# Optimization experiments

Hardware: AMD Instinct MI355X
Metric: run time of the kernel (lower is better)

Reference implementation:

```python
import jax, jax.numpy as jnp
import numpy as np

N = 16384      # total atoms (8 proteins x ~2048)
E = 524288     # N * max_neighbors(32)
B = 8          # graphs
F_IN = 26      # 20 residue types + 6 atom types
D = 128        # node_dim
H = 256        # hidden_dim
OUT = 64       # output_dim
L = 4          # n_layers
N_RBF = 16
CUTOFF = 10.0


def setup_inputs() -> dict:
    key = jax.random.key(0)
    ks = jax.random.split(key, 24)
    s = 0.05
    inp = {
        "positions": jax.random.normal(ks[0], (N, 3), jnp.float32) * 10.0,
        "node_features": jax.random.normal(ks[1], (N, F_IN), jnp.float32),
        "edge_index": jax.random.randint(ks[2], (2, E), 0, N, jnp.int32),
        "batch": jnp.sort(jax.random.randint(ks[3], (N,), 0, B, jnp.int32)),
        # node embedding MLP
        "emb_W1": jax.random.normal(ks[4], (F_IN, D), jnp.float32) * s,
        "emb_b1": jnp.zeros((D,), jnp.float32),
        "emb_W2": jax.random.normal(ks[5], (D, D), jnp.float32) * s,
        "emb_b2": jnp.zeros((D,), jnp.float32),
        # per-layer message MLP: [2D + n_rbf] -> H -> D
        "msg_W1": jax.random.normal(ks[6], (L, 2 * D + N_RBF, H), jnp.float32) * s,
        "msg_b1": jnp.zeros((L, H), jnp.float32),
        "msg_W2": jax.random.normal(ks[7], (L, H, D), jnp.float32) * s,
        "msg_b2": jnp.zeros((L, D), jnp.float32),
        # per-layer update MLP: [2D] -> H -> D (residual)
        "upd_W1": jax.random.normal(ks[8], (L, 2 * D, H), jnp.float32) * s,
        "upd_b1": jnp.zeros((L, H), jnp.float32),
        "upd_W2": jax.random.normal(ks[9], (L, H, D), jnp.float32) * s,
        "upd_b2": jnp.zeros((L, D), jnp.float32),
        # readout MLP: D -> H -> OUT
        "r_W1": jax.random.normal(ks[10], (D, H), jnp.float32) * s,
        "r_b1": jnp.zeros((H,), jnp.float32),
        "r_W2": jax.random.normal(ks[11], (H, OUT), jnp.float32) * s,
        "r_b2": jnp.zeros((OUT,), jnp.float32),
    }
    return inp


def _mlp2(x, W1, b1, W2, b2):
    return jax.nn.silu(x @ W1 + b1) @ W2 + b2


def _edge_rbf(positions, src, dst):
    rel = positions[dst] - positions[src]                      # (E,3)
    d = jnp.sqrt(jnp.sum(rel * rel, axis=-1) + 1e-12)          # (E,)
    centers = jnp.linspace(0.0, CUTOFF, N_RBF, dtype=positions.dtype)
    width = CUTOFF / N_RBF
    rbf = jnp.exp(-((d[:, None] - centers) ** 2) / (2.0 * width * width))  # (E,n_rbf)
    env = 0.5 * (jnp.cos(jnp.pi * d / CUTOFF) + 1.0) * (d < CUTOFF)        # cosine cutoff
    return rbf * env[:, None]


def reference(positions, node_features, edge_index, batch,
              emb_W1, emb_b1, emb_W2, emb_b2,
              msg_W1, msg_b1, msg_W2, msg_b2,
              upd_W1, upd_b1, upd_W2, upd_b2,
              r_W1, r_b1, r_W2, r_b2):
    src, dst = edge_index[0], edge_index[1]
    h = _mlp2(node_features, emb_W1, emb_b1, emb_W2, emb_b2)   # (N,D)
    ef = _edge_rbf(positions, src, dst)                        # (E,n_rbf)
    for i in range(L):
        m_in = jnp.concatenate([h[src], h[dst], ef], axis=-1)  # (E,2D+n_rbf)
        m = _mlp2(m_in, msg_W1[i], msg_b1[i], msg_W2[i], msg_b2[i])  # (E,D)
        agg = jax.ops.segment_sum(m, dst, num_segments=N)      # (N,D)
        u_in = jnp.concatenate([h, agg], axis=-1)              # (N,2D)
        h = h + _mlp2(u_in, upd_W1[i], upd_b1[i], upd_W2[i], upd_b2[i])
    # mean readout per graph
    counts = jax.ops.segment_sum(jnp.ones((N,), h.dtype), batch, num_segments=B)
    g = jax.ops.segment_sum(h, batch, num_segments=B) / jnp.maximum(counts, 1.0)[:, None]
    return _mlp2(g, r_W1, r_b1, r_W2, r_b2)                    # (B,OUT)
```

## Files before the change

### kernel.cpp

```cpp
#include <hip/hip_runtime.h>
#include <math.h>

#define NATOMS 16384
#define NEDGES 524288
#define NLAYERS 4
#define TE 64

typedef __bf16 bf16x8 __attribute__((ext_vector_type(8)));
typedef __bf16 bf16x4 __attribute__((ext_vector_type(4)));
typedef __bf16 bf16x2 __attribute__((ext_vector_type(2)));
typedef float f32x4 __attribute__((ext_vector_type(4)));

__device__ __forceinline__ float silu_f(float x) {
  return x * __builtin_amdgcn_rcpf(1.0f + __expf(-x));
}

__global__ __launch_bounds__(256) void hist_kernel(
    const int* __restrict__ dst, int* __restrict__ counts)
{
  int e = blockIdx.x * 256 + threadIdx.x;
  atomicAdd(&counts[dst[e]], 1);
}

__global__ __launch_bounds__(1024) void scan_kernel(
    const int* __restrict__ counts, int* __restrict__ cursor,
    float* __restrict__ degf)
{
  __shared__ int s_tot[1024];
  int tid = threadIdx.x;
  int v[16];
  {
    const int4* cp = (const int4*)(counts + tid * 16);
    int4 a = cp[0], b = cp[1], c = cp[2], d = cp[3];
    v[0]=a.x; v[1]=a.y; v[2]=a.z; v[3]=a.w;
    v[4]=b.x; v[5]=b.y; v[6]=b.z; v[7]=b.w;
    v[8]=c.x; v[9]=c.y; v[10]=c.z; v[11]=c.w;
    v[12]=d.x; v[13]=d.y; v[14]=d.z; v[15]=d.w;
  }
  int tot = 0;
  #pragma unroll
  for (int i = 0; i < 16; i++) tot += v[i];
  s_tot[tid] = tot;
  __syncthreads();
  for (int off = 1; off < 1024; off <<= 1) {
    int t = (tid >= off) ? s_tot[tid - off] : 0;
    __syncthreads();
    s_tot[tid] += t;
    __syncthreads();
  }
  int run = s_tot[tid] - tot;
  #pragma unroll
  for (int i = 0; i < 16; i++) {
    cursor[tid * 16 + i] = run;
    degf[tid * 16 + i] = (float)v[i];
    run += v[i];
  }
}

__global__ __launch_bounds__(256) void scatter_kernel(
    const int* __restrict__ src, const int* __restrict__ dst,
    int* __restrict__ cursor, int* __restrict__ esrc, int* __restrict__ edst)
{
  int e = blockIdx.x * 256 + threadIdx.x;
  int d = dst[e];
  int p = atomicAdd(&cursor[d], 1);
  esrc[p] = src[e];
  edst[p] = d;
}

__global__ __launch_bounds__(256) void prep_kernel(
    const float* __restrict__ mW1, const float* __restrict__ mW2,
    const float* __restrict__ uW1, const float* __restrict__ uW2,
    const float* __restrict__ mb2,
    __bf16* __restrict__ W1at, __bf16* __restrict__ W1bt,
    __bf16* __restrict__ B2c, __bf16* __restrict__ uW1ft,
    __bf16* __restrict__ uW2t, float* __restrict__ b2u)
{
  long l = blockIdx.y;
  int bx = blockIdx.x, tid = threadIdx.x;
  if (bx < 128) {
    int i = bx * 256 + tid;
    int n = i >> 7, k = i & 127;
    W1at[l * (256L * 128) + i] = (__bf16)mW1[l * (272L * 256) + (size_t)k * 256 + n];
  } else if (bx < 256) {
    int i = (bx - 128) * 256 + tid;
    int n = i >> 7, k = i & 127;
    W1bt[l * (256L * 128) + i] = (__bf16)mW1[l * (272L * 256) + (size_t)(128 + k) * 256 + n];
  } else if (bx < 288) {
    int i = (bx - 256) * 256 + tid;
    int c = i >> 5, k = i & 31;
    float v = (k < 16) ? mW1[l * (272L * 256) + (size_t)(256 + k) * 256 + c] : 0.0f;
    B2c[l * (256L * 32) + i] = (__bf16)v;
  } else if (bx < 672) {
    int i = (bx - 288) * 256 + tid;
    int n = i / 384, k = i - n * 384;
    float v;
    if (k < 128) {
      v = uW1[l * 65536 + (size_t)k * 256 + n];
    } else {
      int r = k - 128;
      v = 0.0f;
      for (int j = 0; j < 128; j++)
        v += mW2[(l * 256 + r) * 128 + j] * uW1[l * 65536 + (size_t)(128 + j) * 256 + n];
    }
    uW1ft[l * (256L * 384) + i] = (__bf16)v;
  } else if (bx < 800) {
    int i = (bx - 672) * 256 + tid;
    int n = i >> 8, k = i & 255;
    uW2t[l * (128L * 256) + i] = (__bf16)uW2[l * (256L * 128) + (size_t)k * 128 + n];
  } else {
    int c = tid;
    float acc = 0.0f;
    for (int j = 0; j < 128; j++)
      acc += mb2[l * 128 + j] * uW1[l * 65536 + (size_t)(128 + j) * 256 + c];
    b2u[l * 256 + c] = acc;
  }
}

__global__ __launch_bounds__(128) void embed_kernel(
    const float* __restrict__ x, const float* __restrict__ W1,
    const float* __restrict__ b1, const float* __restrict__ W2,
    const float* __restrict__ b2, float* __restrict__ h,
    __bf16* __restrict__ hb)
{
  int n = blockIdx.x;
  int j = threadIdx.x;
  __shared__ float xs[26];
  __shared__ float hid[128];
  if (j < 26) xs[j] = x[n * 26 + j];
  __syncthreads();
  float acc = b1[j];
  #pragma unroll
  for (int k = 0; k < 26; k++) acc += xs[k] * W1[k * 128 + j];
  hid[j] = silu_f(acc);
  __syncthreads();
  float acc2 = b2[j];
  #pragma unroll 8
  for (int k = 0; k < 128; k++) acc2 += hid[k] * W2[k * 128 + j];
  h[(size_t)n * 128 + j] = acc2;
  hb[(size_t)n * 128 + j] = (__bf16)acc2;
}

__global__ __launch_bounds__(256) void rbf_kernel(
    const float* __restrict__ pos, const int* __restrict__ esrc,
    const int* __restrict__ edst, __bf16* __restrict__ efb)
{
  int e = blockIdx.x * 256 + threadIdx.x;
  int s = esrc[e], d = edst[e];
  float dx = pos[d * 3 + 0] - pos[s * 3 + 0];
  float dy = pos[d * 3 + 1] - pos[s * 3 + 1];
  float dz = pos[d * 3 + 2] - pos[s * 3 + 2];
  float dist = sqrtf(dx * dx + dy * dy + dz * dz + 1e-12f);
  float env = (dist < 10.0f)
                  ? 0.5f * (cosf(3.14159265358979f * dist * 0.1f) + 1.0f)
                  : 0.0f;
  bf16x8 o0, o1;
  #pragma unroll
  for (int i = 0; i < 16; i++) {
    float c = (10.0f / 15.0f) * (float)i;
    float t = dist - c;
    float v = env * __expf(-t * t * 1.28f);
    if (i < 8) o0[i] = (__bf16)v; else o1[i - 8] = (__bf16)v;
  }
  *(bf16x8*)(efb + (size_t)e * 16 + 0) = o0;
  *(bf16x8*)(efb + (size_t)e * 16 + 8) = o1;
}

__global__ __launch_bounds__(256) void zprep_kernel(
    const __bf16* __restrict__ hb, const float* __restrict__ b1,
    const __bf16* __restrict__ W1at, const __bf16* __restrict__ W1bt,
    __bf16* __restrict__ z1b, __bf16* __restrict__ z2b, float* __restrict__ aggH)
{
  __shared__ __bf16 s_n[64][136];
  int tid = threadIdx.x, n0 = blockIdx.x * 64;
  {
    int n = tid >> 2, t4 = tid & 3;
    const bf16x8* hr = (const bf16x8*)(hb + (size_t)(n0 + n) * 128);
    #pragma unroll
    for (int i = 0; i < 4; i++)
      *(bf16x8*)&s_n[n][t4 * 8 + 32 * i] = hr[t4 + 4 * i];
  }
  {
    float4 zz = make_float4(0.f, 0.f, 0.f, 0.f);
    float4* ap = (float4*)(aggH + (size_t)n0 * 256);
    for (int i = tid; i < 64 * 256 / 4; i += 256) ap[i] = zz;
  }
  __syncthreads();
  const int wv = tid >> 6, ln = tid & 63, lc = ln & 15, qd = ln >> 4;
  for (int cp = 0; cp < 2; cp++) {
    f32x4 aA[4][2], aB[4][2];
    #pragma unroll
    for (int nt = 0; nt < 2; nt++) {
      float bv = b1[cp * 128 + wv * 32 + nt * 16 + lc];
      #pragma unroll
      for (int mt = 0; mt < 4; mt++) {
        aA[mt][nt][0] = 0.f; aA[mt][nt][1] = 0.f;
        aA[mt][nt][2] = 0.f; aA[mt][nt][3] = 0.f;
        aB[mt][nt][0] = bv; aB[mt][nt][1] = bv;
        aB[mt][nt][2] = bv; aB[mt][nt][3] = bv;
      }
    }
    #pragma unroll
    for (int kt = 0; kt < 4; kt++) {
      bf16x8 af[4];
      #pragma unroll
      for (int mt = 0; mt < 4; mt++)
        af[mt] = *(const bf16x8*)&s_n[mt * 16 + lc][kt * 32 + qd * 8];
      bf16x8 bwA[2], bwB[2];
      #pragma unroll
      for (int nt = 0; nt < 2; nt++) {
        int c = cp * 128 + wv * 32 + nt * 16 + lc;
        bwA[nt] = *(const bf16x8*)(W1at + (size_t)c * 128 + kt * 32 + qd * 8);
        bwB[nt] = *(const bf16x8*)(W1bt + (size_t)c * 128 + kt * 32 + qd * 8);
      }
      #pragma unroll
      for (int mt = 0; mt < 4; mt++)
        #pragma unroll
        for (int nt = 0; nt < 2; nt++) {
          aA[mt][nt] = __builtin_amdgcn_mfma_f32_16x16x32_bf16(af[mt], bwA[nt], aA[mt][nt], 0, 0, 0);
          aB[mt][nt] = __builtin_amdgcn_mfma_f32_16x16x32_bf16(af[mt], bwB[nt], aB[mt][nt], 0, 0, 0);
        }
    }
    #pragma unroll
    for (int mt = 0; mt < 4; mt++)
      #pragma unroll
      for (int nt = 0; nt < 2; nt++) {
        int c = cp * 128 + wv * 32 + nt * 16 + lc;
        #pragma unroll
        for (int r = 0; r < 4; r++) {
          int n = n0 + mt * 16 + qd * 4 + r;
          z1b[(size_t)n * 256 + c] = (__bf16)aA[mt][nt][r];
          z2b[(size_t)n * 256 + c] = (__bf16)aB[mt][nt][r];
        }
      }
  }
}

#define MS_EF_OFF   33792
#define MS_SRC_OFF  36864
#define MS_DST_OFF  37120
#define MS_MASK_OFF 37376
#define MS_BYTES    37392

__global__ __launch_bounds__(256, 4) void msg_mfma_kernel(
    const __bf16* __restrict__ z1b, const __bf16* __restrict__ z2b,
    const __bf16* __restrict__ efb,
    const int* __restrict__ esrc, const int* __restrict__ edst,
    const __bf16* __restrict__ B2c, float* __restrict__ aggH)
{
  __shared__ __align__(16) char smem[MS_BYTES];
  __bf16 (*s_hT)[66] = (__bf16(*)[66])(smem);
  __bf16 (*s_ef)[24] = (__bf16(*)[24])(smem + MS_EF_OFF);
  int* s_src = (int*)(smem + MS_SRC_OFF);
  int* s_dst = (int*)(smem + MS_DST_OFF);
  unsigned int* s_mask = (unsigned int*)(smem + MS_MASK_OFF);

  int tid = threadIdx.x, e0 = blockIdx.x * TE;

  if (tid < TE) {
    int d = edst[e0 + tid];
    s_dst[tid] = d;
    int dp = (tid == 0) ? (d ^ 1) : edst[e0 + tid - 1];
    unsigned long long mb = __ballot(d != dp);
    if (tid == 0) { s_mask[0] = (unsigned int)mb; s_mask[1] = (unsigned int)(mb >> 32); }
  } else if (tid < 2 * TE) {
    s_src[tid - TE] = esrc[e0 + tid - TE];
  }
  {
    int e = tid >> 2, t4 = tid & 3;
    if (t4 < 2)
      *(bf16x8*)&s_ef[e][t4 * 8] =
          *(const bf16x8*)(efb + (size_t)(e0 + e) * 16 + t4 * 8);
  }
  __syncthreads();

  const int wv = tid >> 6, ln = tid & 63, lc = ln & 15, qd = ln >> 4;

  bf16x8 bI;
  #pragma unroll
  for (int j = 0; j < 8; j++)
    bI[j] = (__bf16)((lc == (qd & 1) * 8 + j) ? 1.0f : 0.0f);

  const __bf16* pz[4];
  #pragma unroll
  for (int mt = 0; mt < 4; mt++) {
    int m = mt * 16 + lc;
    int row = (qd < 2) ? s_src[m] : s_dst[m];
    pz[mt] = ((qd < 2) ? z1b : z2b) + (size_t)row * 256 + (qd & 1) * 8;
  }

  #pragma unroll
  for (int hf = 0; hf < 2; hf++) {
    const int cb = hf * 128 + wv * 32;
    bf16x8 bw[2];
    #pragma unroll
    for (int nt = 0; nt < 2; nt++)
      bw[nt] = *(const bf16x8*)(B2c + (size_t)(cb + nt * 16 + lc) * 32 + qd * 8);

    #pragma unroll
    for (int mt = 0; mt < 4; mt++) {
      bf16x8 aef = *(const bf16x8*)&s_ef[mt * 16 + lc][(qd & 1) * 8];
      #pragma unroll
      for (int nt = 0; nt < 2; nt++) {
        bf16x8 az = *(const bf16x8*)(pz[mt] + cb + nt * 16);
        f32x4 z; z[0] = 0.f; z[1] = 0.f; z[2] = 0.f; z[3] = 0.f;
        f32x4 acc = __builtin_amdgcn_mfma_f32_16x16x32_bf16(az, bI, z, 0, 0, 0);
        acc = __builtin_amdgcn_mfma_f32_16x16x32_bf16(aef, bw[nt], acc, 0, 0, 0);
        bf16x2 p0, p1;
        p0[0] = (__bf16)silu_f(acc[0]); p0[1] = (__bf16)silu_f(acc[1]);
        p1[0] = (__bf16)silu_f(acc[2]); p1[1] = (__bf16)silu_f(acc[3]);
        __bf16* wp = &s_hT[cb + nt * 16 + lc][mt * 16 + qd * 4];
        *(bf16x2*)wp = p0;
        *(bf16x2*)(wp + 2) = p1;
      }
    }
  }
  __syncthreads();

  {
    const unsigned int mlo = __builtin_amdgcn_readfirstlane(s_mask[0]);
    const unsigned int mhi = __builtin_amdgcn_readfirstlane(s_mask[1]);
    int j = tid;
    float acc = 0.0f;
    int cur = s_dst[0];
    #pragma unroll 8
    for (int i = 0; i < 64; i += 2) {
      bf16x2 p = *(const bf16x2*)&s_hT[j][i];
      bool b0 = (i < 32) ? ((mlo >> i) & 1u) : ((mhi >> (i - 32)) & 1u);
      int i1 = i + 1;
      bool b1 = (i1 < 32) ? ((mlo >> i1) & 1u) : ((mhi >> (i1 - 32)) & 1u);
      if (i > 0 && b0) {
        atomicAdd(&aggH[(size_t)cur * 256 + j], acc);
        acc = 0.0f; cur = s_dst[i];
      }
      acc += (float)p[0];
      if (b1) {
        atomicAdd(&aggH[(size_t)cur * 256 + j], acc);
        acc = 0.0f; cur = s_dst[i1];
      }
      acc += (float)p[1];
    }
    atomicAdd(&aggH[(size_t)cur * 256 + j], acc);
  }
}

__global__ __launch_bounds__(256, 2) void upd_mfma_kernel(
    float* __restrict__ h, __bf16* __restrict__ hb,
    float* __restrict__ aggH, const float* __restrict__ degf,
    const __bf16* __restrict__ uW1ft, const float* __restrict__ b1,
    const float* __restrict__ b2u,
    const __bf16* __restrict__ uW2t, const float* __restrict__ b2,
    int do_z, const float* __restrict__ nb1,
    const __bf16* __restrict__ nW1at, const __bf16* __restrict__ nW1bt,
    __bf16* __restrict__ z1b, __bf16* __restrict__ z2b)
{
  __shared__ __bf16 s_u[64][392];
  __shared__ __bf16 s_uh[64][136];
  int tid = threadIdx.x, n0 = blockIdx.x * 64;
  {
    int n = tid >> 2, t4 = tid & 3;
    const bf16x8* hr = (const bf16x8*)(hb + (size_t)(n0 + n) * 128);
    #pragma unroll
    for (int i = 0; i < 4; i++)
      *(bf16x8*)&s_u[n][t4 * 8 + 32 * i] = hr[t4 + 4 * i];
    const float* sr = aggH + (size_t)(n0 + n) * 256;
    #pragma unroll
    for (int i = 0; i < 8; i++) {
      int col = t4 * 8 + i * 32;
      float4 a = *(const float4*)(sr + col);
      float4 b = *(const float4*)(sr + col + 4);
      bf16x8 o;
      o[0] = (__bf16)a.x; o[1] = (__bf16)a.y; o[2] = (__bf16)a.z; o[3] = (__bf16)a.w;
      o[4] = (__bf16)b.x; o[5] = (__bf16)b.y; o[6] = (__bf16)b.z; o[7] = (__bf16)b.w;
      *(bf16x8*)&s_u[n][128 + col] = o;
    }
  }
  __syncthreads();
  const int wv = tid >> 6, ln = tid & 63, lc = ln & 15, qd = ln >> 4;

  float dg[4][4];
  #pragma unroll
  for (int mt = 0; mt < 4; mt++)
    #pragma unroll
    for (int r = 0; r < 4; r++)
      dg[mt][r] = degf[n0 + mt * 16 + qd * 4 + r];

  f32x4 acc2[4][2];
  #pragma unroll
  for (int nt = 0; nt < 2; nt++) {
    float bv = b2[wv * 32 + nt * 16 + lc];
    #pragma unroll
    for (int mt = 0; mt < 4; mt++) {
      acc2[mt][nt][0] = bv; acc2[mt][nt][1] = bv;
      acc2[mt][nt][2] = bv; acc2[mt][nt][3] = bv;
    }
  }

  for (int hf = 0; hf < 2; hf++) {
    f32x4 acc1[4][2];
    #pragma unroll
    for (int nt = 0; nt < 2; nt++) {
      int c = hf * 128 + wv * 32 + nt * 16 + lc;
      float bv = b1[c];
      float b2uv = b2u[c];
      #pragma unroll
      for (int mt = 0; mt < 4; mt++)
        #pragma unroll
        for (int r = 0; r < 4; r++)
          acc1[mt][nt][r] = bv + dg[mt][r] * b2uv;
    }
    #pragma unroll
    for (int kt = 0; kt < 12; kt++) {
      bf16x8 af[4];
      #pragma unroll
      for (int mt = 0; mt < 4; mt++)
        af[mt] = *(const bf16x8*)&s_u[mt * 16 + lc][kt * 32 + qd * 8];
      bf16x8 bw[2];
      #pragma unroll
      for (int nt = 0; nt < 2; nt++)
        bw[nt] = *(const bf16x8*)(uW1ft +
                 (size_t)(hf * 128 + wv * 32 + nt * 16 + lc) * 384 + kt * 32 + qd * 8);
      #pragma unroll
      for (int mt = 0; mt < 4; mt++)
        #pragma unroll
        for (int nt = 0; nt < 2; nt++)
          acc1[mt][nt] = __builtin_amdgcn_mfma_f32_16x16x32_bf16(af[mt], bw[nt], acc1[mt][nt], 0, 0, 0);
    }
    __syncthreads();
    #pragma unroll
    for (int mt = 0; mt < 4; mt++)
      #pragma unroll
      for (int nt = 0; nt < 2; nt++) {
        int cc = wv * 32 + nt * 16 + lc;
        #pragma unroll
        for (int r = 0; r < 4; r++)
          s_uh[mt * 16 + qd * 4 + r][cc] = (__bf16)silu_f(acc1[mt][nt][r]);
      }
    __syncthreads();
    #pragma unroll
    for (int kt = 0; kt < 4; kt++) {
      bf16x8 a2[4];
      #pragma unroll
      for (int mt = 0; mt < 4; mt++)
        a2[mt] = *(const bf16x8*)&s_uh[mt * 16 + lc][kt * 32 + qd * 8];
      bf16x8 b2w[2];
      #pragma unroll
      for (int nt = 0; nt < 2; nt++)
        b2w[nt] = *(const bf16x8*)(uW2t +
                  (size_t)(wv * 32 + nt * 16 + lc) * 256 + hf * 128 + kt * 32 + qd * 8);
      #pragma unroll
      for (int mt = 0; mt < 4; mt++)
        #pragma unroll
        for (int nt = 0; nt < 2; nt++)
          acc2[mt][nt] = __builtin_amdgcn_mfma_f32_16x16x32_bf16(a2[mt], b2w[nt], acc2[mt][nt], 0, 0, 0);
    }
  }

  #pragma unroll
  for (int mt = 0; mt < 4; mt++)
    #pragma unroll
    for (int nt = 0; nt < 2; nt++) {
      int c = wv * 32 + nt * 16 + lc;
      #pragma unroll
      for (int r = 0; r < 4; r++) {
        int n = n0 + mt * 16 + qd * 4 + r;
        float v = h[(size_t)n * 128 + c] + acc2[mt][nt][r];
        h[(size_t)n * 128 + c] = v;
        hb[(size_t)n * 128 + c] = (__bf16)v;
      }
    }

  if (do_z) {
    __syncthreads();
    {
      float4 zz = make_float4(0.f, 0.f, 0.f, 0.f);
      float4* ap = (float4*)(aggH + (size_t)n0 * 256);
      for (int i = tid; i < 64 * 256 / 4; i += 256) ap[i] = zz;
      int n = tid >> 2, t4 = tid & 3;
      const bf16x8* hr = (const bf16x8*)(hb + (size_t)(n0 + n) * 128);
      #pragma unroll
      for (int i = 0; i < 4; i++)
        *(bf16x8*)&s_u[n][t4 * 8 + 32 * i] = hr[t4 + 4 * i];
    }
    __syncthreads();
    for (int cp = 0; cp < 2; cp++) {
      f32x4 aA[4][2], aB[4][2];
      #pragma unroll
      for (int nt = 0; nt < 2; nt++) {
        float bv = nb1[cp * 128 + wv * 32 + nt * 16 + lc];
        #pragma unroll
        for (int mt = 0; mt < 4; mt++) {
          aA[mt][nt][0] = 0.f; aA[mt][nt][1] = 0.f;
          aA[mt][nt][2] = 0.f; aA[mt][nt][3] = 0.f;
          aB[mt][nt][0] = bv; aB[mt][nt][1] = bv;
          aB[mt][nt][2] = bv; aB[mt][nt][3] = bv;
        }
      }
      #pragma unroll
      for (int kt = 0; kt < 4; kt++) {
        bf16x8 af[4];
        #pragma unroll
        for (int mt = 0; mt < 4; mt++)
          af[mt] = *(const bf16x8*)&s_u[mt * 16 + lc][kt * 32 + qd * 8];
        bf16x8 bwA[2], bwB[2];
        #pragma unroll
        for (int nt = 0; nt < 2; nt++) {
          int c = cp * 128 + wv * 32 + nt * 16 + lc;
          bwA[nt] = *(const bf16x8*)(nW1at + (size_t)c * 128 + kt * 32 + qd * 8);
          bwB[nt] = *(const bf16x8*)(nW1bt + (size_t)c * 128 + kt * 32 + qd * 8);
        }
        #pragma unroll
        for (int mt = 0; mt < 4; mt++)
          #pragma unroll
          for (int nt = 0; nt < 2; nt++) {
            aA[mt][nt] = __builtin_amdgcn_mfma_f32_16x16x32_bf16(af[mt], bwA[nt], aA[mt][nt], 0, 0, 0);
            aB[mt][nt] = __builtin_amdgcn_mfma_f32_16x16x32_bf16(af[mt], bwB[nt], aB[mt][nt], 0, 0, 0);
          }
      }
      #pragma unroll
      for (int mt = 0; mt < 4; mt++)
        #pragma unroll
        for (int nt = 0; nt < 2; nt++) {
          int c = cp * 128 + wv * 32 + nt * 16 + lc;
          #pragma unroll
          for (int r = 0; r < 4; r++) {
            int n = n0 + mt * 16 + qd * 4 + r;
            z1b[(size_t)n * 256 + c] = (__bf16)aA[mt][nt][r];
            z2b[(size_t)n * 256 + c] = (__bf16)aB[mt][nt][r];
          }
        }
    }
  }
}

__global__ __launch_bounds__(128) void readout_sum_kernel(
    const float* __restrict__ h, const int* __restrict__ batch,
    float* __restrict__ gsum, float* __restrict__ gcnt)
{
  int j = threadIdx.x;
  int n0 = blockIdx.x * 128;
  float acc = 0.f, cacc = 0.f;
  int cur = batch[n0];
  for (int i = 0; i < 128; i++) {
    int b = batch[n0 + i];
    if (b != cur) {
      atomicAdd(&gsum[cur * 128 + j], acc);
      if (j == 0) atomicAdd(&gcnt[cur], cacc);
      acc = 0.f; cacc = 0.f; cur = b;
    }
    acc += h[(size_t)(n0 + i) * 128 + j];
    cacc += 1.f;
  }
  atomicAdd(&gsum[cur * 128 + j], acc);
  if (j == 0) atomicAdd(&gcnt[cur], cacc);
}

__global__ __launch_bounds__(256) void readout_mlp_kernel(
    const float* __restrict__ gsum, const float* __restrict__ gcnt,
    const float* __restrict__ W1, const float* __restrict__ b1,
    const float* __restrict__ W2, const float* __restrict__ b2,
    float* __restrict__ out)
{
  __shared__ float g[8][128];
  __shared__ float hid[8][256];
  int tid = threadIdx.x;
  for (int i = tid; i < 8 * 128; i += 256) {
    int b = i >> 7, c = i & 127;
    g[b][c] = gsum[i] / fmaxf(gcnt[b], 1.0f);
  }
  __syncthreads();
  {
    float bb = b1[tid];
    float a[8];
    #pragma unroll
    for (int b = 0; b < 8; b++) a[b] = bb;
    for (int k = 0; k < 128; k++) {
      float w = W1[k * 256 + tid];
      #pragma unroll
      for (int b = 0; b < 8; b++) a[b] += g[b][k] * w;
    }
    #pragma unroll
    for (int b = 0; b < 8; b++) hid[b][tid] = silu_f(a[b]);
  }
  __syncthreads();
  int j = tid & 63, bg = tid >> 6;
  float a0 = b2[j], a1 = b2[j];
  for (int k = 0; k < 256; k++) {
    float w = W2[k * 64 + j];
    a0 += hid[bg * 2 + 0][k] * w;
    a1 += hid[bg * 2 + 1][k] * w;
  }
  out[(bg * 2 + 0) * 64 + j] = a0;
  out[(bg * 2 + 1) * 64 + j] = a1;
}

extern "C" void kernel_launch(void* const* d_in, const int* in_sizes, int n_in,
                              void* d_out, int out_size, void* d_ws, size_t ws_size,
                              hipStream_t stream) {
  const float* pos   = (const float*)d_in[0];
  const float* xfeat = (const float*)d_in[1];
  const int*   eidx  = (const int*)d_in[2];
  const int*   batch = (const int*)d_in[3];
  const float* eW1 = (const float*)d_in[4];
  const float* eb1 = (const float*)d_in[5];
  const float* eW2 = (const float*)d_in[6];
  const float* eb2 = (const float*)d_in[7];
  const float* mW1 = (const float*)d_in[8];
  const float* mb1 = (const float*)d_in[9];
  const float* mW2 = (const float*)d_in[10];
  const float* mb2 = (const float*)d_in[11];
  const float* uW1 = (const float*)d_in[12];
  const float* ub1 = (const float*)d_in[13];
  const float* uW2 = (const float*)d_in[14];
  const float* ub2 = (const float*)d_in[15];
  const float* rW1 = (const float*)d_in[16];
  const float* rb1 = (const float*)d_in[17];
  const float* rW2 = (const float*)d_in[18];
  const float* rb2 = (const float*)d_in[19];

  const int* srcI = eidx;
  const int* dstI = eidx + NEDGES;

  char* base = (char*)d_ws;
  float* h    = (float*)base;  base += (size_t)NATOMS * 128 * 4;
  float* aggH = (float*)base;  base += (size_t)NATOMS * 256 * 4;
  __bf16* z1b = (__bf16*)base; base += (size_t)NATOMS * 256 * 2;
  __bf16* z2b = (__bf16*)base; base += (size_t)NATOMS * 256 * 2;
  __bf16* hb  = (__bf16*)base; base += (size_t)NATOMS * 128 * 2;
  __bf16* efb = (__bf16*)base; base += (size_t)NEDGES * 16 * 2;
  __bf16* W1at = (__bf16*)base; base += (size_t)NLAYERS * 256 * 128 * 2;
  __bf16* W1bt = (__bf16*)base; base += (size_t)NLAYERS * 256 * 128 * 2;
  __bf16* B2c  = (__bf16*)base; base += (size_t)NLAYERS * 256 * 32 * 2;
  __bf16* uW1ft = (__bf16*)base; base += (size_t)NLAYERS * 256 * 384 * 2;
  __bf16* uW2t = (__bf16*)base; base += (size_t)NLAYERS * 128 * 256 * 2;
  float* b2u  = (float*)base;  base += (size_t)NLAYERS * 256 * 4;
  float* degf = (float*)base;  base += (size_t)NATOMS * 4;
  float* gsum = (float*)base;  base += 8 * 128 * 4;
  float* gcnt = (float*)base;  base += 8 * 4;
  int* counts = (int*)base;    base += (size_t)NATOMS * 4;
  int* cursor = (int*)base;    base += (size_t)NATOMS * 4;
  int* esrc   = (int*)base;    base += (size_t)NEDGES * 4;
  int* edst   = (int*)base;    base += (size_t)NEDGES * 4;

  hipMemsetAsync(counts, 0, NATOMS * sizeof(int), stream);
  hist_kernel<<<NEDGES / 256, 256, 0, stream>>>(dstI, counts);
  scan_kernel<<<1, 1024, 0, stream>>>(counts, cursor, degf);
  scatter_kernel<<<NEDGES / 256, 256, 0, stream>>>(srcI, dstI, cursor, esrc, edst);

  prep_kernel<<<dim3(801, NLAYERS), 256, 0, stream>>>(
      mW1, mW2, uW1, uW2, mb2, W1at, W1bt, B2c, uW1ft, uW2t, b2u);

  embed_kernel<<<NATOMS, 128, 0, stream>>>(xfeat, eW1, eb1, eW2, eb2, h, hb);
  rbf_kernel<<<NEDGES / 256, 256, 0, stream>>>(pos, esrc, edst, efb);

  zprep_kernel<<<NATOMS / 64, 256, 0, stream>>>(
      hb, mb1, W1at, W1bt, z1b, z2b, aggH);

  for (int l = 0; l < NLAYERS; l++) {
    int ln = (l < NLAYERS - 1) ? (l + 1) : l;
    msg_mfma_kernel<<<NEDGES / TE, 256, 0, stream>>>(
        z1b, z2b, efb, esrc, edst,
        B2c + (size_t)l * 256 * 32, aggH);
    upd_mfma_kernel<<<NATOMS / 64, 256, 0, stream>>>(
        h, hb, aggH, degf,
        uW1ft + (size_t)l * 256 * 384, ub1 + (size_t)l * 256,
        b2u + (size_t)l * 256,
        uW2t + (size_t)l * 128 * 256, ub2 + (size_t)l * 128,
        (l < NLAYERS - 1) ? 1 : 0,
        mb1 + (size_t)ln * 256,
        W1at + (size_t)ln * 256 * 128, W1bt + (size_t)ln * 256 * 128,
        z1b, z2b);
  }

  hipMemsetAsync(gsum, 0, (8 * 128 + 8) * sizeof(float), stream);
  readout_sum_kernel<<<NATOMS / 128, 128, 0, stream>>>(h, batch, gsum, gcnt);
  readout_mlp_kernel<<<1, 256, 0, stream>>>(gsum, gcnt, rW1, rb1, rW2, rb2,
                                            (float*)d_out);
}
```

Baseline: 686.3 us.

## Widen update kernel to 512 threads, splitting hidden and output columns across eight waves

The node update kernel goes from 4 to 8 waves per block. The sequential loops over hidden halves and z-column pairs become a per-wave split across the eight waves, and s_uh grows to hold the full 256-wide hidden activation. This removes the serial hf/cp loops and several barriers, and should give more parallelism per 64-node tile across only 256 blocks. In exchange it uses more LDS per block and has fewer MFMA tiles per wave in the second GEMM.

After: 674.9 us. Within noise of the previous version (-1.7%).

```diff
diff --git a/kernel.cpp b/kernel.cpp
--- a/kernel.cpp
+++ b/kernel.cpp
@@ -344,7 +344,7 @@
   }
 }
 
-__global__ __launch_bounds__(256, 2) void upd_mfma_kernel(
+__global__ __launch_bounds__(512, 2) void upd_mfma_kernel(
     float* __restrict__ h, __bf16* __restrict__ hb,
     float* __restrict__ aggH, const float* __restrict__ degf,
     const __bf16* __restrict__ uW1ft, const float* __restrict__ b1,
@@ -355,18 +355,18 @@
     __bf16* __restrict__ z1b, __bf16* __restrict__ z2b)
 {
   __shared__ __bf16 s_u[64][392];
-  __shared__ __bf16 s_uh[64][136];
+  __shared__ __bf16 s_uh[64][264];
   int tid = threadIdx.x, n0 = blockIdx.x * 64;
   {
-    int n = tid >> 2, t4 = tid & 3;
+    int n = tid >> 3, t8 = tid & 7;
     const bf16x8* hr = (const bf16x8*)(hb + (size_t)(n0 + n) * 128);
     #pragma unroll
-    for (int i = 0; i < 4; i++)
-      *(bf16x8*)&s_u[n][t4 * 8 + 32 * i] = hr[t4 + 4 * i];
+    for (int i = 0; i < 2; i++)
+      *(bf16x8*)&s_u[n][t8 * 8 + 64 * i] = hr[t8 + 8 * i];
     const float* sr = aggH + (size_t)(n0 + n) * 256;
     #pragma unroll
-    for (int i = 0; i < 8; i++) {
-      int col = t4 * 8 + i * 32;
+    for (int i = 0; i < 4; i++) {
+      int col = t8 * 8 + i * 64;
       float4 a = *(const float4*)(sr + col);
       float4 b = *(const float4*)(sr + col + 4);
       bf16x8 o;
@@ -385,22 +385,11 @@
     for (int r = 0; r < 4; r++)
       dg[mt][r] = degf[n0 + mt * 16 + qd * 4 + r];
 
-  f32x4 acc2[4][2];
-  #pragma unroll
-  for (int nt = 0; nt < 2; nt++) {
-    float bv = b2[wv * 32 + nt * 16 + lc];
-    #pragma unroll
-    for (int mt = 0; mt < 4; mt++) {
-      acc2[mt][nt][0] = bv; acc2[mt][nt][1] = bv;
-      acc2[mt][nt][2] = bv; acc2[mt][nt][3] = bv;
-    }
-  }
-
-  for (int hf = 0; hf < 2; hf++) {
+  {
     f32x4 acc1[4][2];
     #pragma unroll
     for (int nt = 0; nt < 2; nt++) {
-      int c = hf * 128 + wv * 32 + nt * 16 + lc;
+      int c = wv * 32 + nt * 16 + lc;
       float bv = b1[c];
       float b2uv = b2u[c];
       #pragma unroll
@@ -419,14 +408,13 @@
       #pragma unroll
       for (int nt = 0; nt < 2; nt++)
         bw[nt] = *(const bf16x8*)(uW1ft +
-                 (size_t)(hf * 128 + wv * 32 + nt * 16 + lc) * 384 + kt * 32 + qd * 8);
+                 (size_t)(wv * 32 + nt * 16 + lc) * 384 + kt * 32 + qd * 8);
       #pragma unroll
       for (int mt = 0; mt < 4; mt++)
         #pragma unroll
         for (int nt = 0; nt < 2; nt++)
           acc1[mt][nt] = __builtin_amdgcn_mfma_f32_16x16x32_bf16(af[mt], bw[nt], acc1[mt][nt], 0, 0, 0);
     }
-    __syncthreads();
     #pragma unroll
     for (int mt = 0; mt < 4; mt++)
       #pragma unroll
@@ -436,38 +424,38 @@
         for (int r = 0; r < 4; r++)
           s_uh[mt * 16 + qd * 4 + r][cc] = (__bf16)silu_f(acc1[mt][nt][r]);
       }
-    __syncthreads();
-    #pragma unroll
-    for (int kt = 0; kt < 4; kt++) {
-      bf16x8 a2[4];
-      #pragma unroll
-      for (int mt = 0; mt < 4; mt++)
-        a2[mt] = *(const bf16x8*)&s_uh[mt * 16 + lc][kt * 32 + qd * 8];
-      bf16x8 b2w[2];
-      #pragma unroll
-      for (int nt = 0; nt < 2; nt++)
-        b2w[nt] = *(const bf16x8*)(uW2t +
-                  (size_t)(wv * 32 + nt * 16 + lc) * 256 + hf * 128 + kt * 32 + qd * 8);
-      #pragma unroll
-      for (int mt = 0; mt < 4; mt++)
-        #pragma unroll
-        for (int nt = 0; nt < 2; nt++)
-          acc2[mt][nt] = __builtin_amdgcn_mfma_f32_16x16x32_bf16(a2[mt], b2w[nt], acc2[mt][nt], 0, 0, 0);
-    }
+  }
+  __syncthreads();
+
+  const int ow = wv * 16 + lc;
+  f32x4 acc2[4];
+  {
+    float bv = b2[ow];
+    #pragma unroll
+    for (int mt = 0; mt < 4; mt++) {
+      acc2[mt][0] = bv; acc2[mt][1] = bv; acc2[mt][2] = bv; acc2[mt][3] = bv;
+    }
+  }
+  #pragma unroll
+  for (int kt = 0; kt < 8; kt++) {
+    bf16x8 a2[4];
+    #pragma unroll
+    for (int mt = 0; mt < 4; mt++)
+      a2[mt] = *(const bf16x8*)&s_uh[mt * 16 + lc][kt * 32 + qd * 8];
+    bf16x8 b2w = *(const bf16x8*)(uW2t + (size_t)ow * 256 + kt * 32 + qd * 8);
+    #pragma unroll
+    for (int mt = 0; mt < 4; mt++)
+      acc2[mt] = __builtin_amdgcn_mfma_f32_16x16x32_bf16(a2[mt], b2w, acc2[mt], 0, 0, 0);
   }
 
   #pragma unroll
   for (int mt = 0; mt < 4; mt++)
     #pragma unroll
-    for (int nt = 0; nt < 2; nt++) {
-      int c = wv * 32 + nt * 16 + lc;
-      #pragma unroll
-      for (int r = 0; r < 4; r++) {
-        int n = n0 + mt * 16 + qd * 4 + r;
-        float v = h[(size_t)n * 128 + c] + acc2[mt][nt][r];
-        h[(size_t)n * 128 + c] = v;
-        hb[(size_t)n * 128 + c] = (__bf16)v;
-      }
+    for (int r = 0; r < 4; r++) {
+      int n = n0 + mt * 16 + qd * 4 + r;
+      float v = h[(size_t)n * 128 + ow] + acc2[mt][r];
+      h[(size_t)n * 128 + ow] = v;
+      hb[(size_t)n * 128 + ow] = (__bf16)v;
     }
 
   if (do_z) {
@@ -475,61 +463,59 @@
     {
       float4 zz = make_float4(0.f, 0.f, 0.f, 0.f);
       float4* ap = (float4*)(aggH + (size_t)n0 * 256);
-      for (int i = tid; i < 64 * 256 / 4; i += 256) ap[i] = zz;
-      int n = tid >> 2, t4 = tid & 3;
+      for (int i = tid; i < 64 * 256 / 4; i += 512) ap[i] = zz;
+      int n = tid >> 3, t8 = tid & 7;
       const bf16x8* hr = (const bf16x8*)(hb + (size_t)(n0 + n) * 128);
       #pragma unroll
-      for (int i = 0; i < 4; i++)
-        *(bf16x8*)&s_u[n][t4 * 8 + 32 * i] = hr[t4 + 4 * i];
+      for (int i = 0; i < 2; i++)
+        *(bf16x8*)&s_u[n][t8 * 8 + 64 * i] = hr[t8 + 8 * i];
     }
     __syncthreads();
-    for (int cp = 0; cp < 2; cp++) {
-      f32x4 aA[4][2], aB[4][2];
+    f32x4 aA[4][2], aB[4][2];
+    #pragma unroll
+    for (int nt = 0; nt < 2; nt++) {
+      float bv = nb1[wv * 32 + nt * 16 + lc];
+      #pragma unroll
+      for (int mt = 0; mt < 4; mt++) {
+        aA[mt][nt][0] = 0.f; aA[mt][nt][1] = 0.f;
+        aA[mt][nt][2] = 0.f; aA[mt][nt][3] = 0.f;
+        aB[mt][nt][0] = bv; aB[mt][nt][1] = bv;
+        aB[mt][nt][2] = bv; aB[mt][nt][3] = bv;
+      }
+    }
+    #pragma unroll
+    for (int kt = 0; kt < 4; kt++) {
+      bf16x8 af[4];
+      #pragma unroll
+      for (int mt = 0; mt < 4; mt++)
+        af[mt] = *(const bf16x8*)&s_u[mt * 16 + lc][kt * 32 + qd * 8];
+      bf16x8 bwA[2], bwB[2];
       #pragma unroll
       for (int nt = 0; nt < 2; nt++) {
-        float bv = nb1[cp * 128 + wv * 32 + nt * 16 + lc];
-        #pragma unroll
-        for (int mt = 0; mt < 4; mt++) {
-          aA[mt][nt][0] = 0.f; aA[mt][nt][1] = 0.f;
-          aA[mt][nt][2] = 0.f; aA[mt][nt][3] = 0.f;
-          aB[mt][nt][0] = bv; aB[mt][nt][1] = bv;
-          aB[mt][nt][2] = bv; aB[mt][nt][3] = bv;
-        }
-      }
-      #pragma unroll
-      for (int kt = 0; kt < 4; kt++) {
-        bf16x8 af[4];
-        #pragma unroll
-        for (int mt = 0; mt < 4; mt++)
-          af[mt] = *(const bf16x8*)&s_u[mt * 16 + lc][kt * 32 + qd * 8];
-        bf16x8 bwA[2], bwB[2];
-        #pragma unroll
-        for (int nt = 0; nt < 2; nt++) {
-          int c = cp * 128 + wv * 32 + nt * 16 + lc;
-          bwA[nt] = *(const bf16x8*)(nW1at + (size_t)c * 128 + kt * 32 + qd * 8);
-          bwB[nt] = *(const bf16x8*)(nW1bt + (size_t)c * 128 + kt * 32 + qd * 8);
-        }
-        #pragma unroll
-        for (int mt = 0; mt < 4; mt++)
-          #pragma unroll
-          for (int nt = 0; nt < 2; nt++) {
-            aA[mt][nt] = __builtin_amdgcn_mfma_f32_16x16x32_bf16(af[mt], bwA[nt], aA[mt][nt], 0, 0, 0);
-            aB[mt][nt] = __builtin_amdgcn_mfma_f32_16x16x32_bf16(af[mt], bwB[nt], aB[mt][nt], 0, 0, 0);
-          }
+        int c = wv * 32 + nt * 16 + lc;
+        bwA[nt] = *(const bf16x8*)(nW1at + (size_t)c * 128 + kt * 32 + qd * 8);
+        bwB[nt] = *(const bf16x8*)(nW1bt + (size_t)c * 128 + kt * 32 + qd * 8);
       }
       #pragma unroll
       for (int mt = 0; mt < 4; mt++)
         #pragma unroll
         for (int nt = 0; nt < 2; nt++) {
-          int c = cp * 128 + wv * 32 + nt * 16 + lc;
-          #pragma unroll
-          for (int r = 0; r < 4; r++) {
-            int n = n0 + mt * 16 + qd * 4 + r;
-            z1b[(size_t)n * 256 + c] = (__bf16)aA[mt][nt][r];
-            z2b[(size_t)n * 256 + c] = (__bf16)aB[mt][nt][r];
-          }
+          aA[mt][nt] = __builtin_amdgcn_mfma_f32_16x16x32_bf16(af[mt], bwA[nt], aA[mt][nt], 0, 0, 0);
+          aB[mt][nt] = __builtin_amdgcn_mfma_f32_16x16x32_bf16(af[mt], bwB[nt], aB[mt][nt], 0, 0, 0);
         }
     }
+    #pragma unroll
+    for (int mt = 0; mt < 4; mt++)
+      #pragma unroll
+      for (int nt = 0; nt < 2; nt++) {
+        int c = wv * 32 + nt * 16 + lc;
+        #pragma unroll
+        for (int r = 0; r < 4; r++) {
+          int n = n0 + mt * 16 + qd * 4 + r;
+          z1b[(size_t)n * 256 + c] = (__bf16)aA[mt][nt][r];
+          z2b[(size_t)n * 256 + c] = (__bf16)aB[mt][nt][r];
+        }
+      }
   }
 }
 
@@ -661,7 +647,7 @@
     msg_mfma_kernel<<<NEDGES / TE, 256, 0, stream>>>(
         z1b, z2b, efb, esrc, edst,
         B2c + (size_t)l * 256 * 32, aggH);
-    upd_mfma_kernel<<<NATOMS / 64, 256, 0, stream>>>(
+    upd_mfma_kernel<<<NATOMS / 64, 512, 0, stream>>>(
         h, hb, aggH, degf,
         uW1ft + (size_t)l * 256 * 384, ub1 + (size_t)l * 256,
         b2u + (size_t)l * 256,
```
